# Optimization experiments

Measured on AMD Instinct MI355X. Metric: run time of the kernel, lower is better.

The kernel has to match this reference:

```python
import jax, jax.numpy as jnp
import numpy as np

N_NODES = 50000
N_EDGES = 800000
F_IN = 128
HID = 128
N_CLASSES = 2
N_GRAPHS = 500
NEG_SLOPE = 0.2


def setup_inputs() -> dict:
    key = jax.random.key(0)
    ks = jax.random.split(key, 16)
    inp = {
        "x": jax.random.normal(ks[0], (N_NODES, F_IN), dtype=jnp.float32),
        "edge_index": jax.random.randint(ks[1], (2, N_EDGES), 0, N_NODES, dtype=jnp.int64),
        "batch": jnp.sort(jax.random.randint(ks[2], (N_NODES,), 0, N_GRAPHS, dtype=jnp.int64)),
    }
    dims = [(F_IN, HID), (HID, HID), (HID, HID)]
    for i, (din, dout) in enumerate(dims, start=1):
        s = 1.0 / np.sqrt(din)
        inp[f"W{i}"] = jax.random.uniform(ks[3 * i], (din, dout), minval=-s, maxval=s, dtype=jnp.float32)
        inp[f"a_src{i}"] = jax.random.uniform(ks[3 * i + 1], (dout,), minval=-s, maxval=s, dtype=jnp.float32)
        inp[f"a_dst{i}"] = jax.random.uniform(ks[3 * i + 2], (dout,), minval=-s, maxval=s, dtype=jnp.float32)
        inp[f"b{i}"] = jnp.zeros((dout,), dtype=jnp.float32)
    s = 1.0 / np.sqrt(HID)
    inp["W_lin"] = jax.random.uniform(ks[12], (HID, N_CLASSES), minval=-s, maxval=s, dtype=jnp.float32)
    inp["b_lin"] = jax.random.uniform(ks[13], (N_CLASSES,), minval=-s, maxval=s, dtype=jnp.float32)
    return inp


def gat_conv(x, src, dst, W, a_src, a_dst, b, n_nodes):
    # single-head PyG GATConv (heads=1, concat), self-loops already in src/dst
    h = x @ W                                   # [N, dout]
    alpha_src = h @ a_src                       # [N]
    alpha_dst = h @ a_dst                       # [N]
    e = jax.nn.leaky_relu(alpha_src[src] + alpha_dst[dst], NEG_SLOPE)  # [E]
    # segment softmax over edges grouped by destination node
    m = jax.ops.segment_max(e, dst, num_segments=n_nodes)
    ex = jnp.exp(e - m[dst])
    denom = jax.ops.segment_sum(ex, dst, num_segments=n_nodes)
    alpha = ex / denom[dst]                     # [E]
    out = jax.ops.segment_sum(h[src] * alpha[:, None], dst, num_segments=n_nodes)
    return out + b


def reference(x, edge_index, batch, W1, a_src1, a_dst1, b1, W2, a_src2, a_dst2, b2,
              W3, a_src3, a_dst3, b3, W_lin, b_lin):
    n = x.shape[0]
    loops = jnp.arange(n, dtype=edge_index.dtype)
    src = jnp.concatenate([edge_index[0], loops])
    dst = jnp.concatenate([edge_index[1], loops])

    h = jax.nn.relu(gat_conv(x, src, dst, W1, a_src1, a_dst1, b1, n))
    h = jax.nn.relu(gat_conv(h, src, dst, W2, a_src2, a_dst2, b2, n))
    h = gat_conv(h, src, dst, W3, a_src3, a_dst3, b3, n)

    # global mean pool over graphs
    sums = jax.ops.segment_sum(h, batch, num_segments=N_GRAPHS)       # [G, HID]
    counts = jax.ops.segment_sum(jnp.ones((n,), h.dtype), batch, num_segments=N_GRAPHS)
    pooled = sums / jnp.maximum(counts, 1.0)[:, None]
    # dropout is identity in eval mode
    return pooled @ W_lin + b_lin
```

## Files before the change

kernel.cpp:

```cpp
#include <hip/hip_runtime.h>
#include <math.h>

#define N_NODES  50000
#define N_EDGES  800000
#define FDIM     128
#define N_GRAPHS 500
#define NEG_SLOPE 0.2f
#define EN_TOTAL (N_EDGES + N_NODES)
#define GEMM_TILES (N_NODES / 16)
#define WT_COLS 144
#define PREP_PLANE_BLOCKS 1024
#define PREP_GRID (3 + PREP_PLANE_BLOCKS + 1)
#define BSHIFT 8
#define BWIDTH 256
#define NBUCK ((N_NODES + BWIDTH - 1) / BWIDTH)
#define BIN_BATCH 8192
#define BIN_BLOCKS ((EN_TOTAL + BIN_BATCH - 1) / BIN_BATCH)

typedef short bf16x8 __attribute__((ext_vector_type(8)));
typedef float f32x4 __attribute__((ext_vector_type(4)));

static __device__ __forceinline__ float lrelu(float x) {
    return x >= 0.f ? x : NEG_SLOPE * x;
}
static __device__ __forceinline__ unsigned short f2bf(float v) {
    unsigned int u = __float_as_uint(v);
    u += 0x7fffu + ((u >> 16) & 1u);
    return (unsigned short)(u >> 16);
}
static __device__ __forceinline__ float bf2f(unsigned short s) {
    return __uint_as_float(((unsigned int)s) << 16);
}

__global__ __launch_bounds__(256) void prep_all(
    const float* __restrict__ X,
    const float* __restrict__ W0, const float* __restrict__ W1,
    const float* __restrict__ W2,
    const float* __restrict__ as0, const float* __restrict__ as1,
    const float* __restrict__ as2,
    const float* __restrict__ ad0, const float* __restrict__ ad1,
    const float* __restrict__ ad2,
    unsigned short* __restrict__ WT,
    unsigned short* __restrict__ PHI, unsigned short* __restrict__ PLO,
    int* __restrict__ bcnt)
{
    __shared__ float wa[256];
    const int b = blockIdx.x, tid = threadIdx.x;

    if (b < 3) {
        const float* W  = (b == 0) ? W0  : (b == 1) ? W1  : W2;
        const float* As = (b == 0) ? as0 : (b == 1) ? as1 : as2;
        const float* Ad = (b == 0) ? ad0 : (b == 1) ? ad1 : ad2;
        unsigned short* hi = WT + (size_t)b * 2 * WT_COLS * FDIM;
        unsigned short* lo = hi + WT_COLS * FDIM;
        {
            const int k = tid & 127;
            const float* av = (tid < 128) ? As : Ad;
            float s = 0.f;
            for (int c = 0; c < 128; ++c) s += W[k * FDIM + c] * av[c];
            wa[tid] = s;
        }
        __syncthreads();
        for (int i = tid; i < FDIM * FDIM; i += 256) {
            const int k = i >> 7, c = i & 127;
            const float v = W[i];
            const unsigned short h = f2bf(v);
            hi[c * FDIM + k] = h;
            lo[c * FDIM + k] = f2bf(v - bf2f(h));
        }
        for (int k = tid; k < FDIM; k += 256) {
            const float vs = wa[k], vd = wa[128 + k];
            const unsigned short hs = f2bf(vs), hd = f2bf(vd);
            hi[128 * FDIM + k] = hs; lo[128 * FDIM + k] = f2bf(vs - bf2f(hs));
            hi[129 * FDIM + k] = hd; lo[129 * FDIM + k] = f2bf(vd - bf2f(hd));
        }
        for (int i = tid; i < 14 * FDIM; i += 256) {
            hi[130 * FDIM + i] = 0;
            lo[130 * FDIM + i] = 0;
        }
    } else if (b < 3 + PREP_PLANE_BLOCKS) {
        const int total = N_NODES * FDIM / 4;
        for (int i = (b - 3) * 256 + tid; i < total; i += PREP_PLANE_BLOCKS * 256) {
            const float4 v = ((const float4*)X)[i];
            ushort4 h4, l4;
            h4.x = f2bf(v.x); l4.x = f2bf(v.x - bf2f(h4.x));
            h4.y = f2bf(v.y); l4.y = f2bf(v.y - bf2f(h4.y));
            h4.z = f2bf(v.z); l4.z = f2bf(v.z - bf2f(h4.z));
            h4.w = f2bf(v.w); l4.w = f2bf(v.w - bf2f(h4.w));
            ((ushort4*)PHI)[i] = h4;
            ((ushort4*)PLO)[i] = l4;
        }
    } else {
        if (tid < 256) bcnt[tid] = 0;
    }
}

__global__ __launch_bounds__(256) void gemm_mfma6(
    const unsigned short* __restrict__ PHI, const unsigned short* __restrict__ PLO,
    const unsigned short* __restrict__ WThi, const unsigned short* __restrict__ WTlo,
    unsigned short* __restrict__ Hb, float* __restrict__ asrcN, float* __restrict__ adstN)
{
    __shared__ unsigned short sH[2][16 * 128];
    __shared__ unsigned short sL[2][16 * 128];

    const int tid = threadIdx.x, wv = tid >> 6, lane = tid & 63;
    const int r16 = lane & 15, g = lane >> 4;
    const int t0 = wv * 2;

    bf16x8 bh[2][4], bl[2][4];
    #pragma unroll
    for (int tt = 0; tt < 2; ++tt) {
        const int c = (t0 + tt) * 16 + r16;
        #pragma unroll
        for (int cc = 0; cc < 4; ++cc) {
            bh[tt][cc] = *(const bf16x8*)(WThi + c * FDIM + cc * 32 + 8 * g);
            bl[tt][cc] = *(const bf16x8*)(WTlo + c * FDIM + cc * 32 + 8 * g);
        }
    }
    const unsigned short* WThiE = WThi + (128 + r16) * FDIM + 8 * g;
    const unsigned short* WTloE = WTlo + (128 + r16) * FDIM + 8 * g;

    const int srow = wv * 4 + (lane >> 4);
    const int sslot = lane & 15;
    const int ldsOfs = srow * 128 + ((sslot ^ (srow & 7)) * 8);
    const size_t gOfs0 = (size_t)srow * FDIM + sslot * 8;

    int tile = blockIdx.x;
    {
        const size_t go = (size_t)tile * 16 * FDIM + gOfs0;
        *(uint4*)(&sH[0][ldsOfs]) = *(const uint4*)(PHI + go);
        *(uint4*)(&sL[0][ldsOfs]) = *(const uint4*)(PLO + go);
    }
    __syncthreads();

    int cur = 0, rot = 0;
    for (; tile < GEMM_TILES; tile += gridDim.x, ++rot) {
        const int nxt = tile + (int)gridDim.x;
        if (nxt < GEMM_TILES) {
            const size_t go = (size_t)nxt * 16 * FDIM + gOfs0;
            *(uint4*)(&sH[cur ^ 1][ldsOfs]) = *(const uint4*)(PHI + go);
            *(uint4*)(&sL[cur ^ 1][ldsOfs]) = *(const uint4*)(PLO + go);
        }

        bf16x8 ah[4], al[4];
        #pragma unroll
        for (int cc = 0; cc < 4; ++cc) {
            const int p = (cc * 4 + g) ^ (r16 & 7);
            const int ofs = r16 * 128 + p * 8;
            ah[cc] = *(const bf16x8*)(&sH[cur][ofs]);
            al[cc] = *(const bf16x8*)(&sL[cur][ofs]);
        }

        f32x4 acc0 = {0.f, 0.f, 0.f, 0.f}, acc1 = {0.f, 0.f, 0.f, 0.f};
        #pragma unroll
        for (int cc = 0; cc < 4; ++cc) {
            acc0 = __builtin_amdgcn_mfma_f32_16x16x32_bf16(ah[cc], bh[0][cc], acc0, 0, 0, 0);
            acc1 = __builtin_amdgcn_mfma_f32_16x16x32_bf16(ah[cc], bh[1][cc], acc1, 0, 0, 0);
            acc0 = __builtin_amdgcn_mfma_f32_16x16x32_bf16(al[cc], bh[0][cc], acc0, 0, 0, 0);
            acc1 = __builtin_amdgcn_mfma_f32_16x16x32_bf16(al[cc], bh[1][cc], acc1, 0, 0, 0);
            acc0 = __builtin_amdgcn_mfma_f32_16x16x32_bf16(ah[cc], bl[0][cc], acc0, 0, 0, 0);
            acc1 = __builtin_amdgcn_mfma_f32_16x16x32_bf16(ah[cc], bl[1][cc], acc1, 0, 0, 0);
        }

        const int m0 = tile * 16;
        const int rowb = m0 + 4 * g;
        #pragma unroll
        for (int r = 0; r < 4; ++r) {
            Hb[(size_t)(rowb + r) * FDIM + (t0 + 0) * 16 + r16] = f2bf(acc0[r]);
            Hb[(size_t)(rowb + r) * FDIM + (t0 + 1) * 16 + r16] = f2bf(acc1[r]);
        }

        if (wv == ((tile + rot) & 3)) {
            f32x4 acce = {0.f, 0.f, 0.f, 0.f};
            #pragma unroll
            for (int cc = 0; cc < 4; ++cc) {
                const bf16x8 bhe = *(const bf16x8*)(WThiE + cc * 32);
                const bf16x8 ble = *(const bf16x8*)(WTloE + cc * 32);
                acce = __builtin_amdgcn_mfma_f32_16x16x32_bf16(ah[cc], bhe, acce, 0, 0, 0);
                acce = __builtin_amdgcn_mfma_f32_16x16x32_bf16(al[cc], bhe, acce, 0, 0, 0);
                acce = __builtin_amdgcn_mfma_f32_16x16x32_bf16(ah[cc], ble, acce, 0, 0, 0);
            }
            if (r16 == 0) {
                #pragma unroll
                for (int r = 0; r < 4; ++r) asrcN[rowb + r] = acce[r];
            } else if (r16 == 1) {
                #pragma unroll
                for (int r = 0; r < 4; ++r) adstN[rowb + r] = acce[r];
            }
        }

        __syncthreads();
        cur ^= 1;
    }
}

__global__ __launch_bounds__(256) void bucket_count(const int* __restrict__ ei,
                                                    int* __restrict__ bcnt) {
    __shared__ int hist[NBUCK];
    const int tid = threadIdx.x;
    if (tid < NBUCK) hist[tid] = 0;
    __syncthreads();
    const int i0 = blockIdx.x * BIN_BATCH;
    const int i1 = min(i0 + BIN_BATCH, EN_TOTAL);
    for (int i = i0 + tid; i < i1; i += 256) {
        const int d = (i < N_EDGES) ? ei[N_EDGES + i] : (i - N_EDGES);
        atomicAdd(&hist[d >> BSHIFT], 1);
    }
    __syncthreads();
    if (tid < NBUCK && hist[tid]) atomicAdd(&bcnt[tid], hist[tid]);
}

__global__ __launch_bounds__(256) void bucket_scan(const int* __restrict__ bcnt,
                                                   int* __restrict__ bbase,
                                                   int* __restrict__ bcur,
                                                   int* __restrict__ off) {
    __shared__ int s[256];
    const int tid = threadIdx.x;
    s[tid] = (tid < NBUCK) ? bcnt[tid] : 0;
    __syncthreads();
    #pragma unroll
    for (int d = 1; d < 256; d <<= 1) {
        int t = (tid >= d) ? s[tid - d] : 0;
        __syncthreads();
        s[tid] += t;
        __syncthreads();
    }
    if (tid < NBUCK) {
        const int base = (tid == 0) ? 0 : s[tid - 1];
        bbase[tid] = base;
        bcur[tid] = base;
    }
    if (tid == 0) { bbase[NBUCK] = EN_TOTAL; off[N_NODES] = EN_TOTAL; }
}

__global__ __launch_bounds__(256) void bin_edges(const int* __restrict__ ei,
                                                 int* __restrict__ bcur,
                                                 unsigned int* __restrict__ ebuf) {
    __shared__ int hist[NBUCK], base[NBUCK];
    const int tid = threadIdx.x;
    if (tid < NBUCK) hist[tid] = 0;
    __syncthreads();
    const int i0 = blockIdx.x * BIN_BATCH;
    const int i1 = min(i0 + BIN_BATCH, EN_TOTAL);
    for (int i = i0 + tid; i < i1; i += 256) {
        const int d = (i < N_EDGES) ? ei[N_EDGES + i] : (i - N_EDGES);
        atomicAdd(&hist[d >> BSHIFT], 1);
    }
    __syncthreads();
    if (tid < NBUCK) {
        base[tid] = hist[tid] ? atomicAdd(&bcur[tid], hist[tid]) : 0;
        hist[tid] = 0;
    }
    __syncthreads();
    for (int i = i0 + tid; i < i1; i += 256) {
        int s, d;
        if (i < N_EDGES) { s = ei[i]; d = ei[N_EDGES + i]; }
        else             { s = d = i - N_EDGES; }
        const int b = d >> BSHIFT;
        const int r = atomicAdd(&hist[b], 1);
        ebuf[base[b] + r] = ((unsigned int)(d & (BWIDTH - 1)) << 17) | (unsigned int)s;
    }
}

__global__ __launch_bounds__(512) void place_edges(
    const int* __restrict__ bbase, const unsigned int* __restrict__ ebuf,
    int* __restrict__ off, int* __restrict__ srcs)
{
    __shared__ int hist[BWIDTH], scn[BWIDTH];
    const int b = blockIdx.x, tid = threadIdx.x;
    const int d0 = b << BSHIFT;
    const int nd = min(BWIDTH, N_NODES - d0);
    const int bstart = bbase[b], bend = bbase[b + 1];

    if (tid < BWIDTH) hist[tid] = 0;
    __syncthreads();
    for (int i = bstart + tid; i < bend; i += 512)
        atomicAdd(&hist[ebuf[i] >> 17], 1);
    __syncthreads();
    if (tid < BWIDTH) scn[tid] = hist[tid];
    __syncthreads();
    #pragma unroll
    for (int d = 1; d < BWIDTH; d <<= 1) {
        int t = (tid < BWIDTH && tid >= d) ? scn[tid - d] : 0;
        __syncthreads();
        if (tid < BWIDTH) scn[tid] += t;
        __syncthreads();
    }
    if (tid < nd) {
        const int start = bstart + (tid ? scn[tid - 1] : 0);
        off[d0 + tid] = start;
        hist[tid] = start;
    }
    __syncthreads();
    for (int i = bstart + tid; i < bend; i += 512) {
        const unsigned int e = ebuf[i];
        const int p = atomicAdd(&hist[e >> 17], 1);
        srcs[p] = (int)(e & 0x1FFFFu);
    }
}

__global__ __launch_bounds__(256) void gat_aggregate(
    const unsigned short* __restrict__ Hb, const int* __restrict__ off,
    const int* __restrict__ srcs,
    const float* __restrict__ asrcN, const float* __restrict__ adstN,
    const float* __restrict__ bias,
    unsigned short* __restrict__ PHI, unsigned short* __restrict__ PLO,
    float* __restrict__ OUTF, int mode)
{
    const int wave = threadIdx.x >> 6, lane = threadIdx.x & 63;
    const int grp = lane >> 3, fl = lane & 7;

    for (int n = blockIdx.x * 4 + wave; n < N_NODES; n += gridDim.x * 4) {
        const int s0 = off[n], s1 = off[n + 1];
        const int deg = s1 - s0;
        const float ad = adstN[n];

        float e_reg = -1e30f;
        float m = -1e30f;
        for (int j = s0 + lane; j < s1; j += 64) {
            float e = lrelu(asrcN[srcs[j]] + ad);
            if (j - s0 < 64) e_reg = e;
            m = fmaxf(m, e);
        }
        #pragma unroll
        for (int o = 32; o; o >>= 1) m = fmaxf(m, __shfl_xor(m, o));

        float4 a0 = {0,0,0,0}, a1 = {0,0,0,0}, a2 = {0,0,0,0}, a3 = {0,0,0,0};
        float dn = 0.f;
        const unsigned short* Hf = Hb + (size_t)fl * 16;
        for (int j = s0 + grp; j < s1; j += 8) {
            const int s = srcs[j];
            const float ex = (deg <= 64)
                ? __expf(__shfl(e_reg, j - s0) - m)
                : __expf(lrelu(asrcN[s] + ad) - m);
            dn += ex;
            const uint4* hp = (const uint4*)(Hf + (size_t)s * FDIM);
            const uint4 u0 = hp[0], u1 = hp[1];
            a0.x += ex * __uint_as_float(u0.x << 16);
            a0.y += ex * __uint_as_float(u0.x & 0xffff0000u);
            a0.z += ex * __uint_as_float(u0.y << 16);
            a0.w += ex * __uint_as_float(u0.y & 0xffff0000u);
            a1.x += ex * __uint_as_float(u0.z << 16);
            a1.y += ex * __uint_as_float(u0.z & 0xffff0000u);
            a1.z += ex * __uint_as_float(u0.w << 16);
            a1.w += ex * __uint_as_float(u0.w & 0xffff0000u);
            a2.x += ex * __uint_as_float(u1.x << 16);
            a2.y += ex * __uint_as_float(u1.x & 0xffff0000u);
            a2.z += ex * __uint_as_float(u1.y << 16);
            a2.w += ex * __uint_as_float(u1.y & 0xffff0000u);
            a3.x += ex * __uint_as_float(u1.z << 16);
            a3.y += ex * __uint_as_float(u1.z & 0xffff0000u);
            a3.z += ex * __uint_as_float(u1.w << 16);
            a3.w += ex * __uint_as_float(u1.w & 0xffff0000u);
        }

        #pragma unroll
        for (int o = 8; o <= 32; o <<= 1) {
            dn  += __shfl_xor(dn, o);
            a0.x += __shfl_xor(a0.x, o); a0.y += __shfl_xor(a0.y, o);
            a0.z += __shfl_xor(a0.z, o); a0.w += __shfl_xor(a0.w, o);
            a1.x += __shfl_xor(a1.x, o); a1.y += __shfl_xor(a1.y, o);
            a1.z += __shfl_xor(a1.z, o); a1.w += __shfl_xor(a1.w, o);
            a2.x += __shfl_xor(a2.x, o); a2.y += __shfl_xor(a2.y, o);
            a2.z += __shfl_xor(a2.z, o); a2.w += __shfl_xor(a2.w, o);
            a3.x += __shfl_xor(a3.x, o); a3.y += __shfl_xor(a3.y, o);
            a3.z += __shfl_xor(a3.z, o); a3.w += __shfl_xor(a3.w, o);
        }

        if (grp == 0) {
            const float rd = 1.f / dn;
            const float4* bp = (const float4*)(bias + fl * 16);
            float4 ov[4] = {a0, a1, a2, a3};
            #pragma unroll
            for (int q = 0; q < 4; ++q) {
                const float4 b4 = bp[q];
                float4 o4;
                o4.x = ov[q].x * rd + b4.x; o4.y = ov[q].y * rd + b4.y;
                o4.z = ov[q].z * rd + b4.z; o4.w = ov[q].w * rd + b4.w;
                if (mode == 0) {
                    o4.x = fmaxf(o4.x, 0.f); o4.y = fmaxf(o4.y, 0.f);
                    o4.z = fmaxf(o4.z, 0.f); o4.w = fmaxf(o4.w, 0.f);
                    ushort4 h4, l4;
                    h4.x = f2bf(o4.x); l4.x = f2bf(o4.x - bf2f(h4.x));
                    h4.y = f2bf(o4.y); l4.y = f2bf(o4.y - bf2f(h4.y));
                    h4.z = f2bf(o4.z); l4.z = f2bf(o4.z - bf2f(h4.z));
                    h4.w = f2bf(o4.w); l4.w = f2bf(o4.w - bf2f(h4.w));
                    const size_t base = (size_t)n * FDIM + fl * 16 + q * 4;
                    *(ushort4*)(PHI + base) = h4;
                    *(ushort4*)(PLO + base) = l4;
                } else {
                    *(float4*)(OUTF + (size_t)n * FDIM + fl * 16 + q * 4) = o4;
                }
            }
        }
    }
}

__global__ __launch_bounds__(256) void pool_linear2(
    const float* __restrict__ H, const int* __restrict__ batch,
    const float* __restrict__ Wlin, const float* __restrict__ blin,
    float* __restrict__ out)
{
    const int g = blockIdx.x, tid = threadIdx.x;
    const int rl = tid >> 5, fq = tid & 31;

    int a = 0, b = N_NODES;
    while (a < b) { int mid = (a + b) >> 1; if (batch[mid] < g) a = mid + 1; else b = mid; }
    const int lo = a;
    b = N_NODES;
    while (a < b) { int mid = (a + b) >> 1; if (batch[mid] <= g) a = mid + 1; else b = mid; }
    const int hi = a;

    float4 acc = {0.f, 0.f, 0.f, 0.f};
    for (int n = lo + rl; n < hi; n += 8) {
        const float4 v = *(const float4*)(H + (size_t)n * FDIM + fq * 4);
        acc.x += v.x; acc.y += v.y; acc.z += v.z; acc.w += v.w;
    }
    __shared__ float4 s[8][32];
    s[rl][fq] = acc;
    __syncthreads();

    if (tid < 32) {
        float4 t = s[0][fq];
        #pragma unroll
        for (int r = 1; r < 8; ++r) {
            const float4 v = s[r][fq];
            t.x += v.x; t.y += v.y; t.z += v.z; t.w += v.w;
        }
        const float inv = 1.f / fmaxf((float)(hi - lo), 1.f);
        t.x *= inv; t.y *= inv; t.z *= inv; t.w *= inv;
        float d0 = t.x * Wlin[(fq * 4 + 0) * 2 + 0] + t.y * Wlin[(fq * 4 + 1) * 2 + 0]
                 + t.z * Wlin[(fq * 4 + 2) * 2 + 0] + t.w * Wlin[(fq * 4 + 3) * 2 + 0];
        float d1 = t.x * Wlin[(fq * 4 + 0) * 2 + 1] + t.y * Wlin[(fq * 4 + 1) * 2 + 1]
                 + t.z * Wlin[(fq * 4 + 2) * 2 + 1] + t.w * Wlin[(fq * 4 + 3) * 2 + 1];
        #pragma unroll
        for (int o = 1; o <= 16; o <<= 1) {
            d0 += __shfl_xor(d0, o);
            d1 += __shfl_xor(d1, o);
        }
        if (fq == 0) {
            out[g * 2 + 0] = d0 + blin[0];
            out[g * 2 + 1] = d1 + blin[1];
        }
    }
}

extern "C" void kernel_launch(void* const* d_in, const int* in_sizes, int n_in,
                              void* d_out, int out_size, void* d_ws, size_t ws_size,
                              hipStream_t stream)
{
    const float* x     = (const float*)d_in[0];
    const int*   ei    = (const int*)d_in[1];
    const int*   batch = (const int*)d_in[2];
    const float* W[3]    = {(const float*)d_in[3],  (const float*)d_in[7],  (const float*)d_in[11]};
    const float* avs[3]  = {(const float*)d_in[4],  (const float*)d_in[8],  (const float*)d_in[12]};
    const float* avd[3]  = {(const float*)d_in[5],  (const float*)d_in[9],  (const float*)d_in[13]};
    const float* bias[3] = {(const float*)d_in[6],  (const float*)d_in[10], (const float*)d_in[14]};
    const float* Wlin = (const float*)d_in[15];
    const float* blin = (const float*)d_in[16];
    float* out = (float*)d_out;

    char* w = (char*)d_ws;
    unsigned short* PHI = (unsigned short*)w; w += (size_t)N_NODES * FDIM * 2;
    unsigned short* PLO = (unsigned short*)w; w += (size_t)N_NODES * FDIM * 2;
    float* hOf = (float*)PHI;
    unsigned short* Hb = (unsigned short*)w; w += (size_t)N_NODES * FDIM * 2;
    float* attn  = (float*)w; w += 2 * 200192;
    int*   off   = (int*)w;   w += 200192;
    int*   bcnt  = (int*)w;   w += 1024;
    int*   bbase = (int*)w;   w += 1024;
    int*   bcur  = (int*)w;   w += 1024;
    int*   srcs  = (int*)w;   w += (size_t)EN_TOTAL * 4;
    unsigned int* ebuf = (unsigned int*)w; w += (size_t)EN_TOTAL * 4;
    unsigned short* WT = (unsigned short*)w; w += (size_t)3 * 2 * WT_COLS * FDIM * 2;
    float* asrcN = attn;
    float* adstN = attn + N_NODES;

    prep_all<<<PREP_GRID, 256, 0, stream>>>(x, W[0], W[1], W[2],
                                            avs[0], avs[1], avs[2],
                                            avd[0], avd[1], avd[2],
                                            WT, PHI, PLO, bcnt);

    bucket_count<<<BIN_BLOCKS, 256, 0, stream>>>(ei, bcnt);
    bucket_scan<<<1, 256, 0, stream>>>(bcnt, bbase, bcur, off);
    bin_edges<<<BIN_BLOCKS, 256, 0, stream>>>(ei, bcur, ebuf);
    place_edges<<<NBUCK, 512, 0, stream>>>(bbase, ebuf, off, srcs);

    for (int l = 0; l < 3; ++l) {
        const unsigned short* WThi = WT + (size_t)l * 2 * WT_COLS * FDIM;
        const unsigned short* WTlo = WThi + WT_COLS * FDIM;
        gemm_mfma6<<<1024, 256, 0, stream>>>(PHI, PLO, WThi, WTlo, Hb, asrcN, adstN);
        gat_aggregate<<<2048, 256, 0, stream>>>(Hb, off, srcs, asrcN, adstN, bias[l],
                                                PHI, PLO, hOf, (l < 2) ? 0 : 1);
    }

    pool_linear2<<<N_GRAPHS, 256, 0, stream>>>(hOf, batch, Wlin, blin, out);
}
```

Baseline: 298.7 us.

## Fuse edge bucket counting into prep kernel and launch one GEMM tile per block

```diff
diff --git a/kernel.cpp b/kernel.cpp
--- a/kernel.cpp
+++ b/kernel.cpp
@@ -10,12 +10,12 @@
 #define GEMM_TILES (N_NODES / 16)
 #define WT_COLS 144
 #define PREP_PLANE_BLOCKS 1024
-#define PREP_GRID (3 + PREP_PLANE_BLOCKS + 1)
 #define BSHIFT 8
 #define BWIDTH 256
 #define NBUCK ((N_NODES + BWIDTH - 1) / BWIDTH)
 #define BIN_BATCH 8192
 #define BIN_BLOCKS ((EN_TOTAL + BIN_BATCH - 1) / BIN_BATCH)
+#define PREP_GRID (3 + PREP_PLANE_BLOCKS + BIN_BLOCKS)
 
 typedef short bf16x8 __attribute__((ext_vector_type(8)));
 typedef float f32x4 __attribute__((ext_vector_type(4)));
@@ -33,7 +33,7 @@
 }
 
 __global__ __launch_bounds__(256) void prep_all(
-    const float* __restrict__ X,
+    const float* __restrict__ X, const int* __restrict__ ei,
     const float* __restrict__ W0, const float* __restrict__ W1,
     const float* __restrict__ W2,
     const float* __restrict__ as0, const float* __restrict__ as1,
@@ -42,9 +42,10 @@
     const float* __restrict__ ad2,
     unsigned short* __restrict__ WT,
     unsigned short* __restrict__ PHI, unsigned short* __restrict__ PLO,
-    int* __restrict__ bcnt)
+    int* __restrict__ bcnt_part)
 {
     __shared__ float wa[256];
+    __shared__ int hist[BWIDTH];
     const int b = blockIdx.x, tid = threadIdx.x;
 
     if (b < 3) {
@@ -91,21 +92,41 @@
             ((ushort4*)PLO)[i] = l4;
         }
     } else {
-        if (tid < 256) bcnt[tid] = 0;
-    }
-}
-
-__global__ __launch_bounds__(256) void gemm_mfma6(
+        const int cb = b - 3 - PREP_PLANE_BLOCKS;
+        if (tid < BWIDTH) hist[tid] = 0;
+        __syncthreads();
+        const int i0 = cb * BIN_BATCH;
+        const int i1 = min(i0 + BIN_BATCH, EN_TOTAL);
+        for (int i = i0 + tid; i < i1; i += 256) {
+            const int d = (i < N_EDGES) ? ei[N_EDGES + i] : (i - N_EDGES);
+            atomicAdd(&hist[d >> BSHIFT], 1);
+        }
+        __syncthreads();
+        if (tid < BWIDTH) bcnt_part[cb * BWIDTH + tid] = hist[tid];
+    }
+}
+
+__global__ __launch_bounds__(256) void gemm_mfma8(
     const unsigned short* __restrict__ PHI, const unsigned short* __restrict__ PLO,
     const unsigned short* __restrict__ WThi, const unsigned short* __restrict__ WTlo,
     unsigned short* __restrict__ Hb, float* __restrict__ asrcN, float* __restrict__ adstN)
 {
-    __shared__ unsigned short sH[2][16 * 128];
-    __shared__ unsigned short sL[2][16 * 128];
+    __shared__ unsigned short sH[16 * 128];
+    __shared__ unsigned short sL[16 * 128];
 
     const int tid = threadIdx.x, wv = tid >> 6, lane = tid & 63;
     const int r16 = lane & 15, g = lane >> 4;
     const int t0 = wv * 2;
+    const int tile = blockIdx.x;
+
+    {
+        const int srow = wv * 4 + (lane >> 4);
+        const int sslot = lane & 15;
+        const int ldsOfs = srow * 128 + ((sslot ^ (srow & 7)) * 8);
+        const size_t go = (size_t)tile * 16 * FDIM + (size_t)srow * FDIM + sslot * 8;
+        *(uint4*)(&sH[ldsOfs]) = *(const uint4*)(PHI + go);
+        *(uint4*)(&sL[ldsOfs]) = *(const uint4*)(PLO + go);
+    }
 
     bf16x8 bh[2][4], bl[2][4];
     #pragma unroll
@@ -117,106 +138,67 @@
             bl[tt][cc] = *(const bf16x8*)(WTlo + c * FDIM + cc * 32 + 8 * g);
         }
     }
-    const unsigned short* WThiE = WThi + (128 + r16) * FDIM + 8 * g;
-    const unsigned short* WTloE = WTlo + (128 + r16) * FDIM + 8 * g;
-
-    const int srow = wv * 4 + (lane >> 4);
-    const int sslot = lane & 15;
-    const int ldsOfs = srow * 128 + ((sslot ^ (srow & 7)) * 8);
-    const size_t gOfs0 = (size_t)srow * FDIM + sslot * 8;
-
-    int tile = blockIdx.x;
-    {
-        const size_t go = (size_t)tile * 16 * FDIM + gOfs0;
-        *(uint4*)(&sH[0][ldsOfs]) = *(const uint4*)(PHI + go);
-        *(uint4*)(&sL[0][ldsOfs]) = *(const uint4*)(PLO + go);
-    }
-    __syncthreads();
-
-    int cur = 0, rot = 0;
-    for (; tile < GEMM_TILES; tile += gridDim.x, ++rot) {
-        const int nxt = tile + (int)gridDim.x;
-        if (nxt < GEMM_TILES) {
-            const size_t go = (size_t)nxt * 16 * FDIM + gOfs0;
-            *(uint4*)(&sH[cur ^ 1][ldsOfs]) = *(const uint4*)(PHI + go);
-            *(uint4*)(&sL[cur ^ 1][ldsOfs]) = *(const uint4*)(PLO + go);
-        }
-
-        bf16x8 ah[4], al[4];
+    __syncthreads();
+
+    bf16x8 ah[4], al[4];
+    #pragma unroll
+    for (int cc = 0; cc < 4; ++cc) {
+        const int p = (cc * 4 + g) ^ (r16 & 7);
+        const int ofs = r16 * 128 + p * 8;
+        ah[cc] = *(const bf16x8*)(&sH[ofs]);
+        al[cc] = *(const bf16x8*)(&sL[ofs]);
+    }
+
+    f32x4 acc0 = {0.f, 0.f, 0.f, 0.f}, acc1 = {0.f, 0.f, 0.f, 0.f};
+    #pragma unroll
+    for (int cc = 0; cc < 4; ++cc) {
+        acc0 = __builtin_amdgcn_mfma_f32_16x16x32_bf16(ah[cc], bh[0][cc], acc0, 0, 0, 0);
+        acc1 = __builtin_amdgcn_mfma_f32_16x16x32_bf16(ah[cc], bh[1][cc], acc1, 0, 0, 0);
+        acc0 = __builtin_amdgcn_mfma_f32_16x16x32_bf16(al[cc], bh[0][cc], acc0, 0, 0, 0);
+        acc1 = __builtin_amdgcn_mfma_f32_16x16x32_bf16(al[cc], bh[1][cc], acc1, 0, 0, 0);
+        acc0 = __builtin_amdgcn_mfma_f32_16x16x32_bf16(ah[cc], bl[0][cc], acc0, 0, 0, 0);
+        acc1 = __builtin_amdgcn_mfma_f32_16x16x32_bf16(ah[cc], bl[1][cc], acc1, 0, 0, 0);
+    }
+
+    const int m0 = tile * 16;
+    const int rowb = m0 + 4 * g;
+    #pragma unroll
+    for (int r = 0; r < 4; ++r) {
+        Hb[(size_t)(rowb + r) * FDIM + (t0 + 0) * 16 + r16] = f2bf(acc0[r]);
+        Hb[(size_t)(rowb + r) * FDIM + (t0 + 1) * 16 + r16] = f2bf(acc1[r]);
+    }
+
+    if (wv == (tile & 3)) {
+        const unsigned short* WThiE = WThi + (128 + r16) * FDIM + 8 * g;
+        const unsigned short* WTloE = WTlo + (128 + r16) * FDIM + 8 * g;
+        f32x4 acce = {0.f, 0.f, 0.f, 0.f};
         #pragma unroll
         for (int cc = 0; cc < 4; ++cc) {
-            const int p = (cc * 4 + g) ^ (r16 & 7);
-            const int ofs = r16 * 128 + p * 8;
-            ah[cc] = *(const bf16x8*)(&sH[cur][ofs]);
-            al[cc] = *(const bf16x8*)(&sL[cur][ofs]);
-        }
-
-        f32x4 acc0 = {0.f, 0.f, 0.f, 0.f}, acc1 = {0.f, 0.f, 0.f, 0.f};
-        #pragma unroll
-        for (int cc = 0; cc < 4; ++cc) {
-            acc0 = __builtin_amdgcn_mfma_f32_16x16x32_bf16(ah[cc], bh[0][cc], acc0, 0, 0, 0);
-            acc1 = __builtin_amdgcn_mfma_f32_16x16x32_bf16(ah[cc], bh[1][cc], acc1, 0, 0, 0);
-            acc0 = __builtin_amdgcn_mfma_f32_16x16x32_bf16(al[cc], bh[0][cc], acc0, 0, 0, 0);
-            acc1 = __builtin_amdgcn_mfma_f32_16x16x32_bf16(al[cc], bh[1][cc], acc1, 0, 0, 0);
-            acc0 = __builtin_amdgcn_mfma_f32_16x16x32_bf16(ah[cc], bl[0][cc], acc0, 0, 0, 0);
-            acc1 = __builtin_amdgcn_mfma_f32_16x16x32_bf16(ah[cc], bl[1][cc], acc1, 0, 0, 0);
-        }
-
-        const int m0 = tile * 16;
-        const int rowb = m0 + 4 * g;
-        #pragma unroll
-        for (int r = 0; r < 4; ++r) {
-            Hb[(size_t)(rowb + r) * FDIM + (t0 + 0) * 16 + r16] = f2bf(acc0[r]);
-            Hb[(size_t)(rowb + r) * FDIM + (t0 + 1) * 16 + r16] = f2bf(acc1[r]);
-        }
-
-        if (wv == ((tile + rot) & 3)) {
-            f32x4 acce = {0.f, 0.f, 0.f, 0.f};
+            const bf16x8 bhe = *(const bf16x8*)(WThiE + cc * 32);
+            const bf16x8 ble = *(const bf16x8*)(WTloE + cc * 32);
+            acce = __builtin_amdgcn_mfma_f32_16x16x32_bf16(ah[cc], bhe, acce, 0, 0, 0);
+            acce = __builtin_amdgcn_mfma_f32_16x16x32_bf16(al[cc], bhe, acce, 0, 0, 0);
+            acce = __builtin_amdgcn_mfma_f32_16x16x32_bf16(ah[cc], ble, acce, 0, 0, 0);
+        }
+        if (r16 == 0) {
             #pragma unroll
-            for (int cc = 0; cc < 4; ++cc) {
-                const bf16x8 bhe = *(const bf16x8*)(WThiE + cc * 32);
-                const bf16x8 ble = *(const bf16x8*)(WTloE + cc * 32);
-                acce = __builtin_amdgcn_mfma_f32_16x16x32_bf16(ah[cc], bhe, acce, 0, 0, 0);
-                acce = __builtin_amdgcn_mfma_f32_16x16x32_bf16(al[cc], bhe, acce, 0, 0, 0);
-                acce = __builtin_amdgcn_mfma_f32_16x16x32_bf16(ah[cc], ble, acce, 0, 0, 0);
-            }
-            if (r16 == 0) {
-                #pragma unroll
-                for (int r = 0; r < 4; ++r) asrcN[rowb + r] = acce[r];
-            } else if (r16 == 1) {
-                #pragma unroll
-                for (int r = 0; r < 4; ++r) adstN[rowb + r] = acce[r];
-            }
-        }
-
-        __syncthreads();
-        cur ^= 1;
-    }
-}
-
-__global__ __launch_bounds__(256) void bucket_count(const int* __restrict__ ei,
-                                                    int* __restrict__ bcnt) {
-    __shared__ int hist[NBUCK];
-    const int tid = threadIdx.x;
-    if (tid < NBUCK) hist[tid] = 0;
-    __syncthreads();
-    const int i0 = blockIdx.x * BIN_BATCH;
-    const int i1 = min(i0 + BIN_BATCH, EN_TOTAL);
-    for (int i = i0 + tid; i < i1; i += 256) {
-        const int d = (i < N_EDGES) ? ei[N_EDGES + i] : (i - N_EDGES);
-        atomicAdd(&hist[d >> BSHIFT], 1);
-    }
-    __syncthreads();
-    if (tid < NBUCK && hist[tid]) atomicAdd(&bcnt[tid], hist[tid]);
-}
-
-__global__ __launch_bounds__(256) void bucket_scan(const int* __restrict__ bcnt,
+            for (int r = 0; r < 4; ++r) asrcN[rowb + r] = acce[r];
+        } else if (r16 == 1) {
+            #pragma unroll
+            for (int r = 0; r < 4; ++r) adstN[rowb + r] = acce[r];
+        }
+    }
+}
+
+__global__ __launch_bounds__(256) void bucket_scan(const int* __restrict__ bcnt_part,
                                                    int* __restrict__ bbase,
                                                    int* __restrict__ bcur,
                                                    int* __restrict__ off) {
     __shared__ int s[256];
     const int tid = threadIdx.x;
-    s[tid] = (tid < NBUCK) ? bcnt[tid] : 0;
+    int sum = 0;
+    for (int p = 0; p < BIN_BLOCKS; ++p) sum += bcnt_part[p * BWIDTH + tid];
+    s[tid] = (tid < NBUCK) ? sum : 0;
     __syncthreads();
     #pragma unroll
     for (int d = 1; d < 256; d <<= 1) {
@@ -234,24 +216,19 @@
 }
 
 __global__ __launch_bounds__(256) void bin_edges(const int* __restrict__ ei,
+                                                 const int* __restrict__ bcnt_part,
                                                  int* __restrict__ bcur,
                                                  unsigned int* __restrict__ ebuf) {
     __shared__ int hist[NBUCK], base[NBUCK];
     const int tid = threadIdx.x;
-    if (tid < NBUCK) hist[tid] = 0;
+    if (tid < NBUCK) {
+        const int h = bcnt_part[blockIdx.x * BWIDTH + tid];
+        base[tid] = h ? atomicAdd(&bcur[tid], h) : 0;
+        hist[tid] = 0;
+    }
     __syncthreads();
     const int i0 = blockIdx.x * BIN_BATCH;
     const int i1 = min(i0 + BIN_BATCH, EN_TOTAL);
-    for (int i = i0 + tid; i < i1; i += 256) {
-        const int d = (i < N_EDGES) ? ei[N_EDGES + i] : (i - N_EDGES);
-        atomicAdd(&hist[d >> BSHIFT], 1);
-    }
-    __syncthreads();
-    if (tid < NBUCK) {
-        base[tid] = hist[tid] ? atomicAdd(&bcur[tid], hist[tid]) : 0;
-        hist[tid] = 0;
-    }
-    __syncthreads();
     for (int i = i0 + tid; i < i1; i += 256) {
         int s, d;
         if (i < N_EDGES) { s = ei[i]; d = ei[N_EDGES + i]; }
@@ -324,6 +301,7 @@
         }
         #pragma unroll
         for (int o = 32; o; o >>= 1) m = fmaxf(m, __shfl_xor(m, o));
+        const float ex_reg = (lane < deg) ? __expf(e_reg - m) : 0.f;
 
         float4 a0 = {0,0,0,0}, a1 = {0,0,0,0}, a2 = {0,0,0,0}, a3 = {0,0,0,0};
         float dn = 0.f;
@@ -331,7 +309,7 @@
         for (int j = s0 + grp; j < s1; j += 8) {
             const int s = srcs[j];
             const float ex = (deg <= 64)
-                ? __expf(__shfl(e_reg, j - s0) - m)
+                ? __shfl(ex_reg, j - s0)
                 : __expf(lrelu(asrcN[s] + ad) - m);
             dn += ex;
             const uint4* hp = (const uint4*)(Hf + (size_t)s * FDIM);
@@ -467,7 +445,7 @@
     unsigned short* Hb = (unsigned short*)w; w += (size_t)N_NODES * FDIM * 2;
     float* attn  = (float*)w; w += 2 * 200192;
     int*   off   = (int*)w;   w += 200192;
-    int*   bcnt  = (int*)w;   w += 1024;
+    int*   bcnt_part = (int*)w; w += (size_t)BIN_BLOCKS * BWIDTH * 4;
     int*   bbase = (int*)w;   w += 1024;
     int*   bcur  = (int*)w;   w += 1024;
     int*   srcs  = (int*)w;   w += (size_t)EN_TOTAL * 4;
@@ -476,20 +454,19 @@
     float* asrcN = attn;
     float* adstN = attn + N_NODES;
 
-    prep_all<<<PREP_GRID, 256, 0, stream>>>(x, W[0], W[1], W[2],
+    prep_all<<<PREP_GRID, 256, 0, stream>>>(x, ei, W[0], W[1], W[2],
                                             avs[0], avs[1], avs[2],
                                             avd[0], avd[1], avd[2],
-                                            WT, PHI, PLO, bcnt);
-
-    bucket_count<<<BIN_BLOCKS, 256, 0, stream>>>(ei, bcnt);
-    bucket_scan<<<1, 256, 0, stream>>>(bcnt, bbase, bcur, off);
-    bin_edges<<<BIN_BLOCKS, 256, 0, stream>>>(ei, bcur, ebuf);
+                                            WT, PHI, PLO, bcnt_part);
+
+    bucket_scan<<<1, 256, 0, stream>>>(bcnt_part, bbase, bcur, off);
+    bin_edges<<<BIN_BLOCKS, 256, 0, stream>>>(ei, bcnt_part, bcur, ebuf);
     place_edges<<<NBUCK, 512, 0, stream>>>(bbase, ebuf, off, srcs);
 
     for (int l = 0; l < 3; ++l) {
         const unsigned short* WThi = WT + (size_t)l * 2 * WT_COLS * FDIM;
         const unsigned short* WTlo = WThi + WT_COLS * FDIM;
-        gemm_mfma6<<<1024, 256, 0, stream>>>(PHI, PLO, WThi, WTlo, Hb, asrcN, adstN);
+        gemm_mfma8<<<GEMM_TILES, 256, 0, stream>>>(PHI, PLO, WThi, WTlo, Hb, asrcN, adstN);
         gat_aggregate<<<2048, 256, 0, stream>>>(Hb, off, srcs, asrcN, adstN, bias[l],
                                                 PHI, PLO, hOf, (l < 2) ? 0 : 1);
     }
```

After: 316.9 us. 1.06x slower.
